# Performance work log

Hardware: AMD Instinct MI355X
Metric: run time of the kernel (lower is better)

The kernel has to match this reference:

```python
import jax, jax.numpy as jnp
import numpy as np

D_IN = 1024
D_OUT = 1024
N_HEADS = 16
HEAD_DIM = D_OUT // N_HEADS

def setup_inputs() -> dict:
    key = jax.random.key(0)
    ks = jax.random.split(key, 6)
    s = 0.02
    x = jax.random.normal(ks[0], (2, 2048, D_IN), dtype=jnp.float32)
    Wq = jax.random.normal(ks[1], (D_IN, D_OUT), dtype=jnp.float32) * s
    Wk = jax.random.normal(ks[2], (D_IN, D_OUT), dtype=jnp.float32) * s
    Wv = jax.random.normal(ks[3], (D_IN, D_OUT), dtype=jnp.float32) * s
    Wo = jax.random.normal(ks[4], (D_OUT, D_OUT), dtype=jnp.float32) * s
    bo = jnp.zeros((D_OUT,), dtype=jnp.float32)
    return {"x": x, "Wq": Wq, "Wk": Wk, "Wv": Wv, "Wo": Wo, "bo": bo}

def reference(x, Wq, Wk, Wv, Wo, bo):
    b, t, _ = x.shape
    # project and split heads: [b, h, t, d]
    def split_heads(y):
        return y.reshape(b, t, N_HEADS, HEAD_DIM).transpose(0, 2, 1, 3)
    q = split_heads(x @ Wq)
    k = split_heads(x @ Wk)
    v = split_heads(x @ Wv)
    # NOTE: original code applies NO 1/sqrt(head_dim) scaling
    scores = jnp.einsum('bhqd,bhkd->bhqk', q, k)
    causal = jnp.tril(jnp.ones((t, t), dtype=bool))  # keep lower triangle
    scores = jnp.where(causal, scores, -jnp.inf)
    attn = jax.nn.softmax(scores, axis=-1)
    ctx = jnp.einsum('bhqk,bhkd->bhqd', attn, v)
    ctx = ctx.transpose(0, 2, 1, 3).reshape(b, t, D_OUT)
    return ctx @ Wo + bo
```

## Files before the change

kernel.cpp:

```cpp
#include <hip/hip_runtime.h>

typedef unsigned short u16;
typedef unsigned int   u32;
typedef __bf16 bf16x2 __attribute__((ext_vector_type(2)));
typedef __bf16 bf16x8 __attribute__((ext_vector_type(8)));
typedef float  f32x4  __attribute__((ext_vector_type(4)));
typedef float  f32x16 __attribute__((ext_vector_type(16)));
typedef u32    u32x4  __attribute__((ext_vector_type(4)));

#define LOG2E 1.4426950408889634f

__device__ __forceinline__ u16 f2bf(float f) {
  union { float f; u32 u; } v; v.f = f;
  u32 r = v.u + 0x7fffu + ((v.u >> 16) & 1u);
  return (u16)(r >> 16);
}

__device__ __forceinline__ u32 pack2(float lo, float hi) {
  bf16x2 p = { (__bf16)lo, (__bf16)hi };
  return __builtin_bit_cast(u32, p);
}

#define GLOAD_LDS16(g, s) __builtin_amdgcn_global_load_lds( \
    (const __attribute__((address_space(1))) void*)(g),     \
    (__attribute__((address_space(3))) void*)(s), 16, 0, 0)


__global__ void k_convert(const float* __restrict__ in, u16* __restrict__ out) {
  int i = (blockIdx.x * 256 + threadIdx.x) * 8;
  float4 a = *(const float4*)(in + i);
  float4 b = *(const float4*)(in + i + 4);
  u16 o[8] = { f2bf(a.x), f2bf(a.y), f2bf(a.z), f2bf(a.w),
               f2bf(b.x), f2bf(b.y), f2bf(b.z), f2bf(b.w) };
  *(uint4*)(out + i) = *(const uint4*)o;
}

__global__ void k_transpose_w4(const float* __restrict__ Wq, const float* __restrict__ Wk,
                               const float* __restrict__ Wv, const float* __restrict__ Wo,
                               u16* __restrict__ WqkvT, u16* __restrict__ WoT) {
  const int z = blockIdx.z;
  const float* W = (z == 0) ? Wq : (z == 1) ? Wk : (z == 2) ? Wv : Wo;
  u16* WT = (z < 3) ? (WqkvT + ((size_t)z << 20)) : WoT;
  __shared__ float tile[64][65];
  const int t = threadIdx.x;
  const int n0 = blockIdx.x * 64, k0 = blockIdx.y * 64;
  const int r = t >> 4, c4 = (t & 15) * 4;
  #pragma unroll
  for (int rr = 0; rr < 64; rr += 16) {
    float4 v = *(const float4*)(W + (size_t)(k0 + r + rr) * 1024 + n0 + c4);
    tile[r + rr][c4]     = v.x; tile[r + rr][c4 + 1] = v.y;
    tile[r + rr][c4 + 2] = v.z; tile[r + rr][c4 + 3] = v.w;
  }
  __syncthreads();
  #pragma unroll
  for (int rr = 0; rr < 64; rr += 16) {
    u16 o[4] = { f2bf(tile[c4][r + rr]),     f2bf(tile[c4 + 1][r + rr]),
                 f2bf(tile[c4 + 2][r + rr]), f2bf(tile[c4 + 3][r + rr]) };
    *(ushort4*)(WT + (size_t)(n0 + r + rr) * 1024 + k0 + c4) = *(const ushort4*)o;
  }
}


template<int MODE>
__global__ __launch_bounds__(256) void k_gemm_bt(
    const u16* __restrict__ A, const u16* __restrict__ BT,
    void* __restrict__ Cv, const float* __restrict__ bias,
    int M, int N, int K) {
  __shared__ u16 lA[2][128 * 32];
  __shared__ u16 lB[2][128 * 32];
  const int t = threadIdx.x;
  const int l = t & 63, w = t >> 6;
  const int bM = blockIdx.y * 128, bN = blockIdx.x * 128;
  const int wr = w >> 1, wc = w & 1;
  const int NT = K >> 5;

  f32x4 acc[4][4] = {};

  const int fA  = w * 512 + l * 8;
  const int r0  = fA >> 5;
  const int kc0 = fA & 31;

  auto stage = [&](int buf, int kt) {
    const u16* ga = A  + (size_t)(bM + r0) * K + kt * 32 + kc0;
    const u16* gb = BT + (size_t)(bN + r0) * K + kt * 32 + kc0;
    GLOAD_LDS16(ga, &lA[buf][w * 512]);
    GLOAD_LDS16(gb, &lB[buf][w * 512]);
    GLOAD_LDS16(ga + (size_t)64 * K, &lA[buf][2048 + w * 512]);
    GLOAD_LDS16(gb + (size_t)64 * K, &lB[buf][2048 + w * 512]);
  };

  stage(0, 0);
  __syncthreads();
  int buf = 0;
  for (int kt = 0; kt < NT; ++kt) {
    if (kt + 1 < NT) stage(buf ^ 1, kt + 1);
    bf16x8 af[4], bfr[4];
    #pragma unroll
    for (int m = 0; m < 4; ++m)
      af[m] = *(const bf16x8*)&lA[buf][(wr * 64 + m * 16 + (l & 15)) * 32 + (l >> 4) * 8];
    #pragma unroll
    for (int n = 0; n < 4; ++n)
      bfr[n] = *(const bf16x8*)&lB[buf][(wc * 64 + n * 16 + (l & 15)) * 32 + (l >> 4) * 8];
    #pragma unroll
    for (int m = 0; m < 4; ++m)
      #pragma unroll
      for (int n = 0; n < 4; ++n)
        acc[m][n] = __builtin_amdgcn_mfma_f32_16x16x32_bf16(af[m], bfr[n], acc[m][n], 0, 0, 0);
    __syncthreads();
    buf ^= 1;
  }

  #pragma unroll
  for (int m = 0; m < 4; ++m) {
    #pragma unroll
    for (int n = 0; n < 4; ++n) {
      const int row = bM + wr * 64 + m * 16 + (l >> 4) * 4;
      const int col = bN + wc * 64 + n * 16 + (l & 15);
      if (MODE == 1) {
        #pragma unroll
        for (int i = 0; i < 4; ++i)
          ((float*)Cv)[(size_t)(row + i) * N + col] = acc[m][n][i] + bias[col];
      } else if (MODE == 0) {
        #pragma unroll
        for (int i = 0; i < 4; ++i)
          ((u16*)Cv)[(size_t)(row + i) * N + col] = f2bf(acc[m][n][i]);
      } else {
        const int which = col >> 10;
        const int h  = (col >> 6) & 15;
        const int d  = col & 63;
        const int b  = row >> 11;
        const int bh = b * 16 + h;
        const int tile = (row & 2047) >> 5;
        const int tk = row & 31;
        u16* base = (u16*)Cv + (size_t)which * 4194304 + (size_t)bh * 131072 + tile * 2048;
        if (which == 2) {
          u16 o[4] = { f2bf(acc[m][n][0]), f2bf(acc[m][n][1]),
                       f2bf(acc[m][n][2]), f2bf(acc[m][n][3]) };
          *(ushort4*)(base + d * 32 + tk) = *(const ushort4*)o;
        } else {
          #pragma unroll
          for (int i = 0; i < 4; ++i)
            base[(tk + i) * 64 + d] = f2bf(acc[m][n][i]);
        }
      }
    }
  }
}


__global__ __launch_bounds__(256, 4) void k_attn(
    const u16* __restrict__ qt_, const u16* __restrict__ kt_,
    const u16* __restrict__ vt_, u16* __restrict__ ctx) {
  __shared__ float obuf[4][32][64];
  __shared__ float mbuf[4][32];
  __shared__ float lbuf[4][32];
  __shared__ float sbuf[4][32];
  __shared__ float rbuf[32];

  const int t = threadIdx.x;
  const int l = t & 63, w = t >> 6;
  const int hi = l >> 5, ln = l & 31;
  const int bidx = blockIdx.x;
  const int x = bidx & 7;
  const int bh = x * 4 + ((bidx >> 3) & 3);
  const int j = bidx >> 5;
  const int bb = bh >> 4, h = bh & 15;
  const size_t tokbase = (size_t)bb * 2048;
  const size_t hplane = (size_t)bh * 131072;

  const int B  = 64 - j;
  const int s0 = (65 * w) >> 2, s1 = (65 * (w + 1)) >> 2;

  f32x16 oa = {}, ob = {};
  float m = -__builtin_inff(), lh = 0.f;

  auto process = [&](const u16* kb, const u16* vb, const bf16x8 (&qf)[4], bool diag) {
    bf16x8 kf[4];
    #pragma unroll
    for (int ds = 0; ds < 4; ++ds)
      kf[ds] = *(const bf16x8*)(kb + ln * 64 + ds * 16 + hi * 8);

    f32x16 sc = {};
    #pragma unroll
    for (int ds = 0; ds < 4; ++ds)
      sc = __builtin_amdgcn_mfma_f32_32x32x16_bf16(kf[ds], qf[ds], sc, 0, 0, 0);

    bf16x8 v00 = *(const bf16x8*)(vb + ln * 32 + hi * 8);
    bf16x8 v01 = *(const bf16x8*)(vb + ln * 32 + 16 + hi * 8);
    bf16x8 v10 = *(const bf16x8*)(vb + (ln + 32) * 32 + hi * 8);
    bf16x8 v11 = *(const bf16x8*)(vb + (ln + 32) * 32 + 16 + hi * 8);

    if (diag) {
      #pragma unroll
      for (int r = 0; r < 16; ++r) {
        const int kloc = (r & 3) + 8 * (r >> 2) + 4 * hi;
        if (kloc > ln) sc[r] = -__builtin_inff();
      }
    }

    float pm = sc[0];
    #pragma unroll
    for (int r = 1; r < 16; ++r) pm = fmaxf(pm, sc[r]);
    pm = fmaxf(pm, __shfl_xor(pm, 32));

    if (!__all(pm <= m + 8.0f)) {
      const float mn  = fmaxf(m, pm);
      const float scl = exp2f((m - mn) * LOG2E);
      m = mn;
      lh *= scl;
      #pragma unroll
      for (int r = 0; r < 16; ++r) {
        const float sr = __shfl(scl, (r & 3) + 8 * (r >> 2) + 4 * hi);
        oa[r] *= sr; ob[r] *= sr;
      }
    }

    float ph[16];
    #pragma unroll
    for (int r = 0; r < 16; ++r) ph[r] = exp2f((sc[r] - m) * LOG2E);
    float rs = 0.f;
    #pragma unroll
    for (int r = 0; r < 16; ++r) rs += ph[r];
    lh += rs;

    u32 c0 = pack2(ph[0],  ph[1]),  c1 = pack2(ph[2],  ph[3]);
    u32 c2 = pack2(ph[4],  ph[5]),  c3 = pack2(ph[6],  ph[7]);
    u32 c4 = pack2(ph[8],  ph[9]),  c5 = pack2(ph[10], ph[11]);
    u32 c6 = pack2(ph[12], ph[13]), c7 = pack2(ph[14], ph[15]);
    const u32 q0 = __shfl_xor(c0, 32), q1 = __shfl_xor(c1, 32);
    const u32 q2 = __shfl_xor(c2, 32), q3 = __shfl_xor(c3, 32);
    const u32 q4 = __shfl_xor(c4, 32), q5 = __shfl_xor(c5, 32);
    const u32 q6 = __shfl_xor(c6, 32), q7 = __shfl_xor(c7, 32);
    const bool h0 = (hi == 0);
    u32x4 wa0 = { h0 ? c0 : q2, h0 ? c1 : q3, h0 ? q0 : c2, h0 ? q1 : c3 };
    u32x4 wa1 = { h0 ? c4 : q6, h0 ? c5 : q7, h0 ? q4 : c6, h0 ? q5 : c7 };
    bf16x8 pa0 = __builtin_bit_cast(bf16x8, wa0);
    bf16x8 pa1 = __builtin_bit_cast(bf16x8, wa1);

    oa = __builtin_amdgcn_mfma_f32_32x32x16_bf16(pa0, v00, oa, 0, 0, 0);
    oa = __builtin_amdgcn_mfma_f32_32x32x16_bf16(pa1, v01, oa, 0, 0, 0);
    ob = __builtin_amdgcn_mfma_f32_32x32x16_bf16(pa0, v10, ob, 0, 0, 0);
    ob = __builtin_amdgcn_mfma_f32_32x32x16_bf16(pa1, v11, ob, 0, 0, 0);
  };

  auto stash = [&](int slot) {
    const float lr = lh + __shfl_xor(lh, 32);
    if (hi == 0) { mbuf[slot][ln] = m; lbuf[slot][ln] = lr; }
    #pragma unroll
    for (int r = 0; r < 16; ++r) {
      const int rm = (r & 3) + 8 * (r >> 2) + 4 * hi;
      obuf[slot][rm][ln]      = oa[r];
      obuf[slot][rm][ln + 32] = ob[r];
    }
  };

  auto runChain = [&](int qt, int k0, int k1) {
    if (k0 >= k1) return;
    bf16x8 qf[4];
    const u16* qq = qt_ + hplane + qt * 2048 + ln * 64 + hi * 8;
    #pragma unroll
    for (int ds = 0; ds < 4; ++ds) qf[ds] = *(const bf16x8*)(qq + ds * 16);
    const u16* kb = kt_ + hplane + k0 * 2048;
    const u16* vb = vt_ + hplane + k0 * 2048;
    for (int kt = k0; kt < k1; ++kt) {
      process(kb, vb, qf, kt == qt);
      kb += 2048; vb += 2048;
    }
  };

  auto mergeWrite = [&](int qt) {
    if (t < 32) {
      const int q = t;
      const float m0 = mbuf[0][q], m1 = mbuf[1][q], m2 = mbuf[2][q], m3 = mbuf[3][q];
      const float ms = fmaxf(fmaxf(m0, m1), fmaxf(m2, m3));
      const float f0 = exp2f((m0 - ms) * LOG2E);
      const float f1 = exp2f((m1 - ms) * LOG2E);
      const float f2 = exp2f((m2 - ms) * LOG2E);
      const float f3 = exp2f((m3 - ms) * LOG2E);
      const float ls = f0 * lbuf[0][q] + f1 * lbuf[1][q] + f2 * lbuf[2][q] + f3 * lbuf[3][q];
      sbuf[0][q] = f0; sbuf[1][q] = f1; sbuf[2][q] = f2; sbuf[3][q] = f3;
      rbuf[q] = 1.0f / ls;
    }
    __syncthreads();
    u16* cb = ctx + (tokbase + qt * 32) * 1024 + h * 64;
    #pragma unroll
    for (int k2 = 0; k2 < 8; ++k2) {
      const int idx = t + k2 * 256;
      const int q = idx >> 6, d = idx & 63;
      const float v = sbuf[0][q] * obuf[0][q][d] + sbuf[1][q] * obuf[1][q][d]
                    + sbuf[2][q] * obuf[2][q][d] + sbuf[3][q] * obuf[3][q][d];
      cb[(size_t)q * 1024 + d] = f2bf(v * rbuf[q]);
    }
  };

  runChain(63 - j, s0, (s1 < B) ? s1 : B);
  stash(w);
  oa = f32x16{}; ob = f32x16{}; m = -__builtin_inff(); lh = 0.f;
  runChain(j, ((s0 > B) ? s0 : B) - B, s1 - B);

  __syncthreads();
  mergeWrite(63 - j);
  __syncthreads();
  stash(w);
  __syncthreads();
  mergeWrite(j);
}


extern "C" void kernel_launch(void* const* d_in, const int* in_sizes, int n_in,
                              void* d_out, int out_size, void* d_ws, size_t ws_size,
                              hipStream_t stream) {
  const float* x  = (const float*)d_in[0];
  const float* Wq = (const float*)d_in[1];
  const float* Wk = (const float*)d_in[2];
  const float* Wv = (const float*)d_in[3];
  const float* Wo = (const float*)d_in[4];
  const float* bo = (const float*)d_in[5];
  float* out = (float*)d_out;
  char* ws = (char*)d_ws;

  u16* xb    = (u16*)(ws);
  u16* WqkvT = (u16*)(ws + (8u  << 20));
  u16* WoT   = (u16*)(ws + (14u << 20));
  u16* Qt    = (u16*)(ws + (16u << 20));
  u16* Kt    = (u16*)(ws + (24u << 20));
  u16* Vt    = (u16*)(ws + (32u << 20));
  u16* ctxb  = (u16*)(ws + (40u << 20));

  k_convert<<<2048, 256, 0, stream>>>(x, xb);
  k_transpose_w4<<<dim3(16, 16, 4), 256, 0, stream>>>(Wq, Wk, Wv, Wo, WqkvT, WoT);

  k_gemm_bt<2><<<dim3(24, 32), 256, 0, stream>>>(xb, WqkvT, Qt, nullptr, 4096, 3072, 1024);
  k_attn<<<1024, 256, 0, stream>>>(Qt, Kt, Vt, ctxb);
  k_gemm_bt<1><<<dim3(8, 32), 256, 0, stream>>>(ctxb, WoT, out, bo, 4096, 1024, 1024);
}
```

Before: 124.8 us.

## Prefetch next K tile in attention loop and trim softmax shuffles

```diff
diff --git a/kernel.cpp b/kernel.cpp
--- a/kernel.cpp
+++ b/kernel.cpp
@@ -148,7 +148,7 @@
 }
 
 
-__global__ __launch_bounds__(256, 4) void k_attn(
+__global__ __launch_bounds__(256, 3) void k_attn(
     const u16* __restrict__ qt_, const u16* __restrict__ kt_,
     const u16* __restrict__ vt_, u16* __restrict__ ctx) {
   __shared__ float obuf[4][32][64];
@@ -174,21 +174,23 @@
   f32x16 oa = {}, ob = {};
   float m = -__builtin_inff(), lh = 0.f;
 
-  auto process = [&](const u16* kb, const u16* vb, const bf16x8 (&qf)[4], bool diag) {
-    bf16x8 kf[4];
+  auto loadK = [&](bf16x8 (&kf)[4], const u16* kb) {
     #pragma unroll
     for (int ds = 0; ds < 4; ++ds)
       kf[ds] = *(const bf16x8*)(kb + ln * 64 + ds * 16 + hi * 8);
-
-    f32x16 sc = {};
-    #pragma unroll
-    for (int ds = 0; ds < 4; ++ds)
-      sc = __builtin_amdgcn_mfma_f32_32x32x16_bf16(kf[ds], qf[ds], sc, 0, 0, 0);
-
+  };
+
+  auto process = [&](const bf16x8 (&kf)[4], const u16* vb, const bf16x8 (&qf)[4],
+                     bool diag) {
     bf16x8 v00 = *(const bf16x8*)(vb + ln * 32 + hi * 8);
     bf16x8 v01 = *(const bf16x8*)(vb + ln * 32 + 16 + hi * 8);
     bf16x8 v10 = *(const bf16x8*)(vb + (ln + 32) * 32 + hi * 8);
     bf16x8 v11 = *(const bf16x8*)(vb + (ln + 32) * 32 + 16 + hi * 8);
+
+    f32x16 sc = {};
+    #pragma unroll
+    for (int ds = 0; ds < 4; ++ds)
+      sc = __builtin_amdgcn_mfma_f32_32x32x16_bf16(kf[ds], qf[ds], sc, 0, 0, 0);
 
     if (diag) {
       #pragma unroll
@@ -198,9 +200,12 @@
       }
     }
 
-    float pm = sc[0];
-    #pragma unroll
-    for (int r = 1; r < 16; ++r) pm = fmaxf(pm, sc[r]);
+    float a0 = fmaxf(sc[0], sc[1]),   a1 = fmaxf(sc[2], sc[3]);
+    float a2 = fmaxf(sc[4], sc[5]),   a3 = fmaxf(sc[6], sc[7]);
+    float a4 = fmaxf(sc[8], sc[9]),   a5 = fmaxf(sc[10], sc[11]);
+    float a6 = fmaxf(sc[12], sc[13]), a7 = fmaxf(sc[14], sc[15]);
+    float pm = fmaxf(fmaxf(fmaxf(a0, a1), fmaxf(a2, a3)),
+                     fmaxf(fmaxf(a4, a5), fmaxf(a6, a7)));
     pm = fmaxf(pm, __shfl_xor(pm, 32));
 
     if (!__all(pm <= m + 8.0f)) {
@@ -218,22 +223,23 @@
     float ph[16];
     #pragma unroll
     for (int r = 0; r < 16; ++r) ph[r] = exp2f((sc[r] - m) * LOG2E);
-    float rs = 0.f;
-    #pragma unroll
-    for (int r = 0; r < 16; ++r) rs += ph[r];
-    lh += rs;
+    float b0 = ph[0] + ph[1],   b1 = ph[2] + ph[3];
+    float b2 = ph[4] + ph[5],   b3 = ph[6] + ph[7];
+    float b4 = ph[8] + ph[9],   b5 = ph[10] + ph[11];
+    float b6 = ph[12] + ph[13], b7 = ph[14] + ph[15];
+    lh += ((b0 + b1) + (b2 + b3)) + ((b4 + b5) + (b6 + b7));
 
     u32 c0 = pack2(ph[0],  ph[1]),  c1 = pack2(ph[2],  ph[3]);
     u32 c2 = pack2(ph[4],  ph[5]),  c3 = pack2(ph[6],  ph[7]);
     u32 c4 = pack2(ph[8],  ph[9]),  c5 = pack2(ph[10], ph[11]);
     u32 c6 = pack2(ph[12], ph[13]), c7 = pack2(ph[14], ph[15]);
-    const u32 q0 = __shfl_xor(c0, 32), q1 = __shfl_xor(c1, 32);
-    const u32 q2 = __shfl_xor(c2, 32), q3 = __shfl_xor(c3, 32);
-    const u32 q4 = __shfl_xor(c4, 32), q5 = __shfl_xor(c5, 32);
-    const u32 q6 = __shfl_xor(c6, 32), q7 = __shfl_xor(c7, 32);
     const bool h0 = (hi == 0);
-    u32x4 wa0 = { h0 ? c0 : q2, h0 ? c1 : q3, h0 ? q0 : c2, h0 ? q1 : c3 };
-    u32x4 wa1 = { h0 ? c4 : q6, h0 ? c5 : q7, h0 ? q4 : c6, h0 ? q5 : c7 };
+    const u32 x0 = __shfl_xor(h0 ? c2 : c0, 32);
+    const u32 x1 = __shfl_xor(h0 ? c3 : c1, 32);
+    const u32 x2 = __shfl_xor(h0 ? c6 : c4, 32);
+    const u32 x3 = __shfl_xor(h0 ? c7 : c5, 32);
+    u32x4 wa0 = { h0 ? c0 : x0, h0 ? c1 : x1, h0 ? x0 : c2, h0 ? x1 : c3 };
+    u32x4 wa1 = { h0 ? c4 : x2, h0 ? c5 : x3, h0 ? x2 : c6, h0 ? x3 : c7 };
     bf16x8 pa0 = __builtin_bit_cast(bf16x8, wa0);
     bf16x8 pa1 = __builtin_bit_cast(bf16x8, wa1);
 
@@ -262,9 +268,18 @@
     for (int ds = 0; ds < 4; ++ds) qf[ds] = *(const bf16x8*)(qq + ds * 16);
     const u16* kb = kt_ + hplane + k0 * 2048;
     const u16* vb = vt_ + hplane + k0 * 2048;
-    for (int kt = k0; kt < k1; ++kt) {
-      process(kb, vb, qf, kt == qt);
-      kb += 2048; vb += 2048;
+
+    bf16x8 kA[4], kB[4];
+    loadK(kA, kb);
+    for (int kt = k0; kt < k1; kt += 2) {
+      const bool more1 = (kt + 1 < k1);
+      if (more1) loadK(kB, kb + 2048);
+      process(kA, vb, qf, kt == qt);
+      if (more1) {
+        if (kt + 2 < k1) loadK(kA, kb + 4096);
+        process(kB, vb + 2048, qf, kt + 1 == qt);
+      }
+      kb += 4096; vb += 4096;
     }
   };
 
```

Result: no change. 125.7 us (+0.7%).
